# Kernel tuning notes

Measured on AMD Instinct MI355X. Metric: run time of the kernel, lower is better.

Reference implementation:

```python
import math
import jax, jax.numpy as jnp
import numpy as np

D_MODEL = 1024
D_STATE = 32
DT_MIN = 0.001
DT_MAX = 0.1
SEQ_LEN = 4096


def setup_inputs() -> dict:
    key = jax.random.key(0)
    kB, kC, kdt = jax.random.split(key, 3)
    log_A_real = jnp.full((D_MODEL, D_STATE), math.log(0.5), dtype=jnp.float32)
    A_imag = jnp.broadcast_to(jnp.linspace(0.0, math.pi, D_STATE, dtype=jnp.float32)[None, :],
                              (D_MODEL, D_STATE)).copy()
    B = jax.random.normal(kB, (D_MODEL, D_STATE, 2), dtype=jnp.float32)
    C = jax.random.normal(kC, (D_MODEL, D_STATE, 2), dtype=jnp.float32)
    log_dt = (jax.random.uniform(kdt, (D_MODEL,), dtype=jnp.float32)
              * (math.log(DT_MAX) - math.log(DT_MIN)) + math.log(DT_MIN))
    return {"log_A_real": log_A_real, "A_imag": A_imag, "B": B, "C": C,
            "log_dt": log_dt, "L": SEQ_LEN}


def reference(log_A_real, A_imag, B, C, log_dt, L):
    # ZOH-discretized diagonal SSM kernel: K[d,l] = Re(sum_n C[d,n] B[d,n] A_bar[d,n]^l)
    dt = jax.nn.softplus(log_dt)                      # (d,)
    A_real = -jax.nn.softplus(log_A_real)             # (d,n) forced negative
    A = jax.lax.complex(A_real, A_imag)               # (d,n) complex64
    A_bar = jnp.exp(dt[:, None] * A)                  # (d,n)
    Bc = jax.lax.complex(B[..., 0], B[..., 1])        # (d,n)
    Cc = jax.lax.complex(C[..., 0], C[..., 1])        # (d,n)
    l = jnp.arange(L, dtype=jnp.float32)              # (L,)
    # A_bar^l via exp(l*log(A_bar)); log(A_bar)=dt*A exactly since |dt*A_imag|<pi
    A_pow = jnp.exp((dt[:, None] * A)[:, :, None] * l)  # (d,n,L) Vandermonde
    K = jnp.einsum('dn,dnl->dl', Cc * Bc, A_pow).real   # (d,L)
    return K
```

## Files before the change

### kernel.cpp

```cpp
#include <hip/hip_runtime.h>
#include <math.h>

#define N_STATE 32

typedef _Float16 f16;
typedef f16 f16x8 __attribute__((ext_vector_type(8)));
typedef float f32x4 __attribute__((ext_vector_type(4)));

__device__ __forceinline__ unsigned swz(int row, int byte_in_row) {
  return (unsigned)(((row << 7) + byte_in_row) ^ ((row & 7) << 4));
}

__global__ __launch_bounds__(256) void s4d_mfma_kernel(
    const float* __restrict__ log_A_real,
    const float* __restrict__ A_imag,
    const float* __restrict__ Bp,
    const float* __restrict__ Cp,
    const float* __restrict__ log_dt,
    float* __restrict__ K,
    int L) {
  const int d = blockIdx.x;
  const int tid = threadIdx.x;

  __shared__ float s_wrl2e[N_STATE], s_wirev[N_STATE];
  __shared__ float s_gr[N_STATE], s_gi[N_STATE];
  __shared__ __align__(16) f16 s_U[64 * 64];
  __shared__ __align__(16) f16 s_V[64 * 64];

  if (tid < N_STATE) {
    const int n = tid;
    const int idx = d * N_STATE + n;
    const float dt = log1pf(expf(log_dt[d]));
    const float wr = -dt * log1pf(expf(log_A_real[idx]));
    const float wi = dt * A_imag[idx];
    s_wrl2e[n] = wr * 1.4426950408889634f;
    s_wirev[n] = wi * 0.15915494309189535f;
    const float br = Bp[2 * idx], bi = Bp[2 * idx + 1];
    const float cr = Cp[2 * idx], ci = Cp[2 * idx + 1];
    s_gr[n] = cr * br - ci * bi;
    s_gi[n] = cr * bi + ci * br;
  }
  __syncthreads();

  {
    const int uh = tid >> 7;
    const int idx = tid & 127;
    const int row = idx & 63;
    const int nh = idx >> 6;
    const float sf = uh ? (float)row : (float)(row * 64);
    f16* tab = uh ? s_V : s_U;
    char* base = (char*)tab;
#pragma unroll
    for (int j = 0; j < 16; ++j) {
      const int n = nh * 16 + j;
      const float er = __builtin_amdgcn_exp2f(s_wrl2e[n] * sf);
      const float ph = __builtin_amdgcn_fractf(s_wirev[n] * sf);
      const float cs = __builtin_amdgcn_cosf(ph);
      const float sn = __builtin_amdgcn_sinf(ph);
      const float zr = er * cs, zi = er * sn;
      float u0, u1;
      if (uh == 0) {
        u0 = s_gr[n] * zr - s_gi[n] * zi;
        u1 = -(s_gr[n] * zi + s_gi[n] * zr);
      } else {
        u0 = zr;
        u1 = zi;
      }
      union { f16 h[2]; unsigned u; } pk;
      pk.h[0] = (f16)u0;
      pk.h[1] = (f16)u1;
      *(unsigned*)(base + swz(row, n * 4)) = pk.u;
    }
  }
  __syncthreads();

  const int wid = tid >> 6;
  const int lane = tid & 63;
  const int r = lane & 15;
  const int g = lane >> 4;

  f16x8 afrag[2];
#pragma unroll
  for (int kt = 0; kt < 2; ++kt)
    afrag[kt] = *(const f16x8*)((const char*)s_U +
                                swz(16 * wid + r, kt * 64 + g * 16));

  f32x4 acc[4];
#pragma unroll
  for (int nt = 0; nt < 4; ++nt) acc[nt] = (f32x4){0.f, 0.f, 0.f, 0.f};

#pragma unroll
  for (int nt = 0; nt < 4; ++nt) {
#pragma unroll
    for (int kt = 0; kt < 2; ++kt) {
      const f16x8 bfrag = *(const f16x8*)((const char*)s_V +
                                          swz(16 * nt + r, kt * 64 + g * 16));
      acc[nt] =
          __builtin_amdgcn_mfma_f32_16x16x32_f16(afrag[kt], bfrag, acc[nt], 0, 0, 0);
    }
  }

  float* outd = K + (size_t)d * L;
#pragma unroll
  for (int nt = 0; nt < 4; ++nt) {
#pragma unroll
    for (int rr = 0; rr < 4; ++rr) {
      const int l = (16 * wid + 4 * g + rr) * 64 + 16 * nt + r;
      __builtin_nontemporal_store(acc[nt][rr], outd + l);
    }
  }
}

extern "C" void kernel_launch(void* const* d_in, const int* in_sizes, int n_in,
                              void* d_out, int out_size, void* d_ws,
                              size_t ws_size, hipStream_t stream) {
  const float* log_A_real = (const float*)d_in[0];
  const float* A_imag = (const float*)d_in[1];
  const float* B = (const float*)d_in[2];
  const float* C = (const float*)d_in[3];
  const float* log_dt = (const float*)d_in[4];
  float* K = (float*)d_out;

  const int D = in_sizes[4];
  const int L = out_size / D;

  dim3 grid(D), block(256);
  hipLaunchKernelGGL(s4d_mfma_kernel, grid, block, 0, stream, log_A_real,
                     A_imag, B, C, log_dt, K, L);
}
```

Measured before the change: 11.69 us.

## Transpose MFMA operands for vectorized output stores and pack LDS table writes

The MFMA operand roles are swapped so each lane's four accumulator values are contiguous in l. That lets the epilogue issue one 16-byte nontemporal store per tile instead of four scalar stores, with the sign of the imaginary part moved so the real-part result is unchanged. Table construction now packs two states per 64-bit LDS write, and softplus uses hardware exp2/log intrinsics in place of library expf/log1pf. The intrinsic softplus may lose precision for large-magnitude inputs.

After: 11.80 us. No clear change (+0.9%).

```diff
diff --git a/kernel.cpp b/kernel.cpp
--- a/kernel.cpp
+++ b/kernel.cpp
@@ -9,6 +9,11 @@
 
 __device__ __forceinline__ unsigned swz(int row, int byte_in_row) {
   return (unsigned)(((row << 7) + byte_in_row) ^ ((row & 7) << 4));
+}
+
+__device__ __forceinline__ float softplus_hw(float x) {
+  const float t = __builtin_amdgcn_exp2f(x * 1.4426950408889634f);
+  return 0.6931471805599453f * __builtin_amdgcn_logf(1.0f + t);
 }
 
 __global__ __launch_bounds__(256) void s4d_mfma_kernel(
@@ -30,8 +35,8 @@
   if (tid < N_STATE) {
     const int n = tid;
     const int idx = d * N_STATE + n;
-    const float dt = log1pf(expf(log_dt[d]));
-    const float wr = -dt * log1pf(expf(log_A_real[idx]));
+    const float dt = softplus_hw(log_dt[d]);
+    const float wr = -dt * softplus_hw(log_A_real[idx]);
     const float wi = dt * A_imag[idx];
     s_wrl2e[n] = wr * 1.4426950408889634f;
     s_wirev[n] = wi * 0.15915494309189535f;
@@ -48,28 +53,32 @@
     const int row = idx & 63;
     const int nh = idx >> 6;
     const float sf = uh ? (float)row : (float)(row * 64);
-    f16* tab = uh ? s_V : s_U;
-    char* base = (char*)tab;
+    char* base = (char*)(uh ? s_V : s_U);
 #pragma unroll
-    for (int j = 0; j < 16; ++j) {
-      const int n = nh * 16 + j;
-      const float er = __builtin_amdgcn_exp2f(s_wrl2e[n] * sf);
-      const float ph = __builtin_amdgcn_fractf(s_wirev[n] * sf);
-      const float cs = __builtin_amdgcn_cosf(ph);
-      const float sn = __builtin_amdgcn_sinf(ph);
-      const float zr = er * cs, zi = er * sn;
-      float u0, u1;
-      if (uh == 0) {
-        u0 = s_gr[n] * zr - s_gi[n] * zi;
-        u1 = -(s_gr[n] * zi + s_gi[n] * zr);
-      } else {
-        u0 = zr;
-        u1 = zi;
+    for (int j = 0; j < 16; j += 2) {
+      union { unsigned u32[2]; unsigned long long u64; } pk2;
+#pragma unroll
+      for (int jj = 0; jj < 2; ++jj) {
+        const int n = nh * 16 + j + jj;
+        const float er = __builtin_amdgcn_exp2f(s_wrl2e[n] * sf);
+        const float ph = __builtin_amdgcn_fractf(s_wirev[n] * sf);
+        const float cs = __builtin_amdgcn_cosf(ph);
+        const float sn = __builtin_amdgcn_sinf(ph);
+        const float zr = er * cs, zi = er * sn;
+        float u0, u1;
+        if (uh == 0) {
+          u0 = s_gr[n] * zr - s_gi[n] * zi;
+          u1 = s_gr[n] * zi + s_gi[n] * zr;
+        } else {
+          u0 = zr;
+          u1 = -zi;
+        }
+        union { f16 h[2]; unsigned u; } pk;
+        pk.h[0] = (f16)u0;
+        pk.h[1] = (f16)u1;
+        pk2.u32[jj] = pk.u;
       }
-      union { f16 h[2]; unsigned u; } pk;
-      pk.h[0] = (f16)u0;
-      pk.h[1] = (f16)u1;
-      *(unsigned*)(base + swz(row, n * 4)) = pk.u;
+      *(unsigned long long*)(base + swz(row, (nh * 16 + j) * 4)) = pk2.u64;
     }
   }
   __syncthreads();
@@ -82,7 +91,7 @@
   f16x8 afrag[2];
 #pragma unroll
   for (int kt = 0; kt < 2; ++kt)
-    afrag[kt] = *(const f16x8*)((const char*)s_U +
+    afrag[kt] = *(const f16x8*)((const char*)s_V +
                                 swz(16 * wid + r, kt * 64 + g * 16));
 
   f32x4 acc[4];
@@ -93,21 +102,18 @@
   for (int nt = 0; nt < 4; ++nt) {
 #pragma unroll
     for (int kt = 0; kt < 2; ++kt) {
-      const f16x8 bfrag = *(const f16x8*)((const char*)s_V +
+      const f16x8 bfrag = *(const f16x8*)((const char*)s_U +
                                           swz(16 * nt + r, kt * 64 + g * 16));
-      acc[nt] =
-          __builtin_amdgcn_mfma_f32_16x16x32_f16(afrag[kt], bfrag, acc[nt], 0, 0, 0);
+      acc[nt] = __builtin_amdgcn_mfma_f32_16x16x32_f16(afrag[kt], bfrag,
+                                                       acc[nt], 0, 0, 0);
     }
   }
 
-  float* outd = K + (size_t)d * L;
+  float* outd = K + (size_t)d * L + 16 * wid + 4 * g;
 #pragma unroll
   for (int nt = 0; nt < 4; ++nt) {
-#pragma unroll
-    for (int rr = 0; rr < 4; ++rr) {
-      const int l = (16 * wid + 4 * g + rr) * 64 + 16 * nt + r;
-      __builtin_nontemporal_store(acc[nt][rr], outd + l);
-    }
+    __builtin_nontemporal_store(acc[nt],
+                                (f32x4*)(outd + 64 * (16 * nt + r)));
   }
 }
 
```
